# Kernel tuning notes

Measured on AMD Instinct MI355X. Metric: run time of the kernel, lower is better.

## Reference

```python
import jax, jax.numpy as jnp
import numpy as np

B, S, D = 2, 2048, 4096
H, KVH, HD = 32, 8, 128
ATTN_MULT = 0.08838834764831845
MAX_ATTN = 30.0
ROPE_THETA = 10000.0
MIN_MASKED = -65504.0  # large negative for masked logits


def setup_inputs() -> dict:
    key = jax.random.key(0)
    ks = jax.random.split(key, 5)
    hidden_states = jax.random.normal(ks[0], (B, S, D), dtype=jnp.float32)
    # boolean mask, True = masked (strictly upper triangular -> causal)
    attention_mask = jnp.triu(jnp.ones((S, S), dtype=bool), k=1)[None, None]
    position_ids = jnp.broadcast_to(jnp.arange(S, dtype=jnp.int64)[None], (B, S))
    sc = 0.02
    Wq = jax.random.normal(ks[1], (D, H * HD), dtype=jnp.float32) * sc
    Wk = jax.random.normal(ks[2], (D, KVH * HD), dtype=jnp.float32) * sc
    Wv = jax.random.normal(ks[3], (D, KVH * HD), dtype=jnp.float32) * sc
    Wo = jax.random.normal(ks[4], (H * HD, D), dtype=jnp.float32) * sc
    return {"hidden_states": hidden_states, "attention_mask": attention_mask,
            "position_ids": position_ids, "Wq": Wq, "Wk": Wk, "Wv": Wv, "Wo": Wo}


def _rotate_half(x):
    x1, x2 = jnp.split(x, 2, axis=-1)
    return jnp.concatenate([-x2, x1], axis=-1)


def _rope_cos_sin(position_ids):
    inv_freq = 1.0 / (ROPE_THETA ** (jnp.arange(0, HD, 2, dtype=jnp.float32) / HD))
    freqs = position_ids.astype(jnp.float32)[..., None] * inv_freq  # [B,S,HD/2]
    emb = jnp.concatenate([freqs, freqs], axis=-1)                  # [B,S,HD]
    return jnp.cos(emb)[:, None], jnp.sin(emb)[:, None]             # [B,1,S,HD]


def reference(hidden_states, attention_mask, position_ids, Wq, Wk, Wv, Wo):
    bsz, q_len, _ = hidden_states.shape
    q = (hidden_states @ Wq).reshape(bsz, q_len, H, HD).transpose(0, 2, 1, 3)
    k = (hidden_states @ Wk).reshape(bsz, q_len, KVH, HD).transpose(0, 2, 1, 3)
    v = (hidden_states @ Wv).reshape(bsz, q_len, KVH, HD).transpose(0, 2, 1, 3)

    cos, sin = _rope_cos_sin(position_ids)
    q = q * cos + _rotate_half(q) * sin
    k = k * cos + _rotate_half(k) * sin

    groups = H // KVH  # repeat_kv (GQA)
    k = jnp.repeat(k, groups, axis=1)
    v = jnp.repeat(v, groups, axis=1)

    w = jnp.einsum('bhqd,bhkd->bhqk', q, k).astype(jnp.float32)
    w = w * ATTN_MULT
    w = MAX_ATTN * jnp.tanh(w / MAX_ATTN)  # Grok-1 tanh soft-cap
    w = jnp.where(attention_mask, jnp.float32(MIN_MASKED), w)
    w = jax.nn.softmax(w, axis=-1).astype(q.dtype)

    out = jnp.einsum('bhqk,bhkd->bhqd', w, v)
    out = out.transpose(0, 2, 1, 3).reshape(bsz, q_len, H * HD)
    return out @ Wo
```

## Files before the change

### kernel.cpp

```cpp
#include <hip/hip_runtime.h>
#include <stdint.h>

#define B_ 2
#define S_ 2048
#define D_ 4096
#define H_ 32
#define KVH_ 8
#define HD_ 128
#define QKVN 6144
#define OHD 4096
#define ATTN_MULT 0.08838834764831845f
#define MAX_ATTN 30.0f

typedef __attribute__((ext_vector_type(8))) short short8;
typedef __attribute__((ext_vector_type(4))) float f32x4;

__device__ __forceinline__ unsigned short f2bf(float x) {
  union { float f; uint32_t u; } v; v.f = x;
  uint32_t r = v.u + 0x7FFFu + ((v.u >> 16) & 1u);
  return (unsigned short)(r >> 16);
}
__device__ __forceinline__ float bf2f(unsigned short h) {
  union { uint32_t u; float f; } v; v.u = ((uint32_t)h) << 16;
  return v.f;
}
__device__ __forceinline__ uint32_t packbf(float lo, float hi) {
  return (uint32_t)f2bf(lo) | ((uint32_t)f2bf(hi) << 16);
}

__global__ void k_cstab(float2* cs) {
  int idx = blockIdx.x * 256 + threadIdx.x;
  int d = idx & 63, s = idx >> 6;
  const float L2_10000 = 13.287712379549449f;
  float inv = exp2f(-(float)d * (L2_10000 / 64.0f));
  float f = (float)s * inv;
  cs[idx] = make_float2(cosf(f), sinf(f));
}

__global__ void k_cvt(const float* __restrict__ x, unsigned short* __restrict__ y, int n4) {
  int i = blockIdx.x * blockDim.x + threadIdx.x;
  int stride = gridDim.x * blockDim.x;
  for (; i < n4; i += stride) {
    float4 v = ((const float4*)x)[i];
    ushort4 o;
    o.x = f2bf(v.x); o.y = f2bf(v.y); o.z = f2bf(v.z); o.w = f2bf(v.w);
    ((ushort4*)y)[i] = o;
  }
}

__global__ void k_transpose(const float* __restrict__ W, unsigned short* __restrict__ WT,
                            int K, int N) {
  __shared__ float tile[32][33];
  int n0 = blockIdx.x * 32, k0 = blockIdx.y * 32;
  int tx = threadIdx.x, ty = threadIdx.y;
#pragma unroll
  for (int j = 0; j < 4; j++)
    tile[ty + j * 8][tx] = W[(size_t)(k0 + ty + j * 8) * N + n0 + tx];
  __syncthreads();
#pragma unroll
  for (int j = 0; j < 4; j++)
    WT[(size_t)(n0 + ty + j * 8) * K + k0 + tx] = f2bf(tile[tx][ty + j * 8]);
}

__global__ void k_rope(unsigned short* __restrict__ qkv, const float2* __restrict__ cs) {
  int row = blockIdx.x;
  int t = blockIdx.y * 256 + threadIdx.x;
  int head = t >> 6, d = t & 63;
  int col = head < H_ ? head * HD_ + d : D_ + (head - H_) * HD_ + d;
  unsigned short* p = qkv + (size_t)row * QKVN + col;
  int s = row & (S_ - 1);
  float2 c = cs[s * 64 + d];
  float x1 = bf2f(p[0]), x2 = bf2f(p[64]);
  p[0]  = f2bf(x1 * c.x - x2 * c.y);
  p[64] = f2bf(x2 * c.x + x1 * c.y);
}

template <bool OUT_BF16>
__global__ __launch_bounds__(256) void k_gemm(const unsigned short* __restrict__ A,
                                              const unsigned short* __restrict__ Bt,
                                              void* __restrict__ Cout,
                                              int M, int N, int K) {
  __shared__ unsigned short As[128 * 32];
  __shared__ unsigned short Bs[128 * 32];
  const int tid = threadIdx.x;
  const int wv = tid >> 6, lane = tid & 63;
  const int lg = lane >> 4, lq = lane & 15;
  const int bm = blockIdx.y * 128, bn = blockIdx.x * 128;
  const int wm = (wv >> 1) * 64, wn = (wv & 1) * 64;
  const int r0 = wv * 16 + (lane >> 2);
  const int kk = (lane & 3) * 8;

  f32x4 acc[4][4] = {};

  for (int k0 = 0; k0 < K; k0 += 32) {
#pragma unroll
    for (int p = 0; p < 2; p++) {
      int r = p * 64 + r0;
      __builtin_amdgcn_global_load_lds(
          (const __attribute__((address_space(1))) void*)(A + (size_t)(bm + r) * K + k0 + kk),
          (__attribute__((address_space(3))) void*)((char*)As + p * 4096 + wv * 1024),
          16, 0, 0);
      __builtin_amdgcn_global_load_lds(
          (const __attribute__((address_space(1))) void*)(Bt + (size_t)(bn + r) * K + k0 + kk),
          (__attribute__((address_space(3))) void*)((char*)Bs + p * 4096 + wv * 1024),
          16, 0, 0);
    }
    __syncthreads();
    short8 a[4], b[4];
#pragma unroll
    for (int f = 0; f < 4; f++) {
      a[f] = *(const short8*)&As[(wm + f * 16 + lq) * 32 + lg * 8];
      b[f] = *(const short8*)&Bs[(wn + f * 16 + lq) * 32 + lg * 8];
    }
#pragma unroll
    for (int i = 0; i < 4; i++)
#pragma unroll
      for (int j = 0; j < 4; j++)
        acc[i][j] = __builtin_amdgcn_mfma_f32_16x16x32_bf16(a[i], b[j], acc[i][j], 0, 0, 0);
    __syncthreads();
  }

#pragma unroll
  for (int i = 0; i < 4; i++)
#pragma unroll
    for (int j = 0; j < 4; j++) {
      int row = bm + wm + i * 16 + lg * 4;
      int col = bn + wn + j * 16 + lq;
#pragma unroll
      for (int t = 0; t < 4; t++) {
        float v = acc[i][j][t];
        if (OUT_BF16)
          ((unsigned short*)Cout)[(size_t)(row + t) * N + col] = f2bf(v);
        else
          ((float*)Cout)[(size_t)(row + t) * N + col] = v;
      }
    }
}

__device__ __forceinline__ float softcap(float s) {
  float x = s * (ATTN_MULT / MAX_ATTN);
  x = fminf(fmaxf(x, -15.f), 15.f);
  float e = __expf(2.0f * x);
  return MAX_ATTN * ((e - 1.0f) / (e + 1.0f));
}

__global__ __launch_bounds__(64) void k_attn(const unsigned short* __restrict__ qkv,
                                             unsigned short* __restrict__ out) {
  const int lane = threadIdx.x;
  const int lg = lane >> 4, lq = lane & 15;
  const int q0 = blockIdx.x * 32;
  const int h = blockIdx.y;
  const int b = blockIdx.z;
  const int kh = h >> 2;

  const unsigned short* Qb = qkv + (size_t)(b * S_) * QKVN + h * HD_;
  const unsigned short* Kb = qkv + (size_t)(b * S_) * QKVN + D_ + kh * HD_;
  const unsigned short* Vb = qkv + (size_t)(b * S_) * QKVN + D_ + KVH_ * HD_ + kh * HD_;

  short8 qf[2][4];
#pragma unroll
  for (int u = 0; u < 2; u++)
#pragma unroll
    for (int c = 0; c < 4; c++)
      qf[u][c] = *(const short8*)(Qb + (size_t)(q0 + u * 16 + lq) * QKVN + c * 32 + lg * 8);

  float m[2] = {-1e30f, -1e30f}, l[2] = {0.f, 0.f};
  f32x4 o[2][8] = {};

  const int kv_end = q0 + 32;
  for (int kv0 = 0; kv0 < kv_end; kv0 += 32) {
    short8 ka[2][4];
#pragma unroll
    for (int sI = 0; sI < 2; sI++)
#pragma unroll
      for (int c = 0; c < 4; c++)
        ka[sI][c] = *(const short8*)(Kb + (size_t)(kv0 + sI * 16 + lq) * QKVN + c * 32 + lg * 8);

    short8 vf[8];
#pragma unroll
    for (int fd = 0; fd < 8; fd++)
#pragma unroll
      for (int j = 0; j < 8; j++)
        vf[fd][j] = (short)Vb[(size_t)(kv0 + lg * 8 + j) * QKVN + fd * 16 + lq];

#pragma unroll
    for (int u = 0; u < 2; u++) {
      f32x4 stA = {}, stB = {};
#pragma unroll
      for (int c = 0; c < 4; c++) {
        stA = __builtin_amdgcn_mfma_f32_16x16x32_bf16(ka[0][c], qf[u][c], stA, 0, 0, 0);
        stB = __builtin_amdgcn_mfma_f32_16x16x32_bf16(ka[1][c], qf[u][c], stB, 0, 0, 0);
      }
      const int gq = q0 + u * 16 + lq;
      float w[8];
#pragma unroll
      for (int i = 0; i < 4; i++) {
        w[i]     = (kv0 + lg * 4 + i > gq)      ? -1e30f : softcap(stA[i]);
        w[4 + i] = (kv0 + 16 + lg * 4 + i > gq) ? -1e30f : softcap(stB[i]);
      }
      float mt = w[0];
#pragma unroll
      for (int i = 1; i < 8; i++) mt = fmaxf(mt, w[i]);
      mt = fmaxf(mt, __shfl_xor(mt, 16));
      mt = fmaxf(mt, __shfl_xor(mt, 32));
      float mnew = fmaxf(m[u], mt);
      float scale = __expf(m[u] - mnew);
      float p[8], ps = 0.f;
#pragma unroll
      for (int i = 0; i < 8; i++) { p[i] = __expf(w[i] - mnew); ps += p[i]; }
      ps += __shfl_xor(ps, 16);
      ps += __shfl_xor(ps, 32);
      l[u] = l[u] * scale + ps;
      m[u] = mnew;

      float sc[4];
#pragma unroll
      for (int t = 0; t < 4; t++)
        sc[t] = __shfl(scale, (lane & 48) + lg * 4 + t, 64);
#pragma unroll
      for (int fd = 0; fd < 8; fd++)
#pragma unroll
        for (int t = 0; t < 4; t++) o[u][fd][t] *= sc[t];

      uint32_t a01 = packbf(p[0], p[1]), a23 = packbf(p[2], p[3]);
      uint32_t b01 = packbf(p[4], p[5]), b23 = packbf(p[6], p[7]);
      int g0 = (lg & 1) << 1;
      int src0 = (g0 << 4) | lq;
      int src1 = ((g0 + 1) << 4) | lq;
      uint32_t wA0 = __shfl(a01, src0, 64), wB0 = __shfl(b01, src0, 64);
      uint32_t wA1 = __shfl(a23, src0, 64), wB1 = __shfl(b23, src0, 64);
      uint32_t wA2 = __shfl(a01, src1, 64), wB2 = __shfl(b01, src1, 64);
      uint32_t wA3 = __shfl(a23, src1, 64), wB3 = __shfl(b23, src1, 64);
      bool useB = lg >= 2;
      union { short8 v; uint32_t w4[4]; } pa;
      pa.w4[0] = useB ? wB0 : wA0;
      pa.w4[1] = useB ? wB1 : wA1;
      pa.w4[2] = useB ? wB2 : wA2;
      pa.w4[3] = useB ? wB3 : wA3;
#pragma unroll
      for (int fd = 0; fd < 8; fd++)
        o[u][fd] = __builtin_amdgcn_mfma_f32_16x16x32_bf16(pa.v, vf[fd], o[u][fd], 0, 0, 0);
    }
  }

#pragma unroll
  for (int u = 0; u < 2; u++) {
    float li[4];
#pragma unroll
    for (int t = 0; t < 4; t++)
      li[t] = __shfl(l[u], (lane & 48) + lg * 4 + t, 64);
#pragma unroll
    for (int fd = 0; fd < 8; fd++)
#pragma unroll
      for (int t = 0; t < 4; t++) {
        int row = q0 + u * 16 + lg * 4 + t;
        int col = h * HD_ + fd * 16 + lq;
        out[(size_t)(b * S_ + row) * OHD + col] = f2bf(o[u][fd][t] / li[t]);
      }
  }
}

extern "C" void kernel_launch(void* const* d_in, const int* in_sizes, int n_in,
                              void* d_out, int out_size, void* d_ws, size_t ws_size,
                              hipStream_t stream) {
  const float* hs = (const float*)d_in[0];
  const float* Wq = (const float*)d_in[3];
  const float* Wk = (const float*)d_in[4];
  const float* Wv = (const float*)d_in[5];
  const float* Wo = (const float*)d_in[6];

  char* ws = (char*)d_ws;
  unsigned short* WqkvT = (unsigned short*)ws;
  unsigned short* hsb   = (unsigned short*)(ws + 50331648);
  float2* cs            = (float2*)(ws + 50331648 + 33554432);
  unsigned short* qkv   = (unsigned short*)d_out;
  unsigned short* WoT   = WqkvT;
  unsigned short* attn  = hsb;

  k_cstab<<<dim3((S_ * 64) / 256), 256, 0, stream>>>(cs);
  k_transpose<<<dim3(4096 / 32, 4096 / 32), dim3(32, 8), 0, stream>>>(Wq, WqkvT, 4096, 4096);
  k_transpose<<<dim3(1024 / 32, 4096 / 32), dim3(32, 8), 0, stream>>>(Wk, WqkvT + (size_t)4096 * 4096, 4096, 1024);
  k_transpose<<<dim3(1024 / 32, 4096 / 32), dim3(32, 8), 0, stream>>>(Wv, WqkvT + (size_t)5120 * 4096, 4096, 1024);
  k_cvt<<<2048, 256, 0, stream>>>(hs, hsb, (B_ * S_ * D_) / 4);
  k_gemm<true><<<dim3(QKVN / 128, (B_ * S_) / 128), 256, 0, stream>>>(hsb, WqkvT, qkv, B_ * S_, QKVN, D_);
  k_rope<<<dim3(B_ * S_, 10), 256, 0, stream>>>(qkv, cs);
  k_transpose<<<dim3(4096 / 32, 4096 / 32), dim3(32, 8), 0, stream>>>(Wo, WoT, 4096, 4096);
  k_attn<<<dim3(S_ / 32, H_, B_), 64, 0, stream>>>(qkv, attn);
  k_gemm<false><<<dim3(D_ / 128, (B_ * S_) / 128), 256, 0, stream>>>(attn, WoT, d_out, B_ * S_, D_, D_);
}
```

Measured before the change: 1.287 ms.

## Transpose V for vector loads, use fixed softcap max, reverse causal block order

```diff
diff --git a/kernel.cpp b/kernel.cpp
--- a/kernel.cpp
+++ b/kernel.cpp
@@ -60,6 +60,22 @@
 #pragma unroll
   for (int j = 0; j < 4; j++)
     WT[(size_t)(n0 + ty + j * 8) * K + k0 + tx] = f2bf(tile[tx][ty + j * 8]);
+}
+
+__global__ void k_vt(const unsigned short* __restrict__ qkv, unsigned short* __restrict__ vT) {
+  __shared__ unsigned short tile[32][34];
+  int c0 = blockIdx.x * 32;
+  int s0 = blockIdx.y * 32;
+  int b  = blockIdx.z;
+  int tx = threadIdx.x, ty = threadIdx.y;
+#pragma unroll
+  for (int j = 0; j < 4; j++)
+    tile[ty + j * 8][tx] =
+        qkv[(size_t)(b * S_ + s0 + ty + j * 8) * QKVN + D_ + KVH_ * HD_ + c0 + tx];
+  __syncthreads();
+#pragma unroll
+  for (int j = 0; j < 4; j++)
+    vT[(size_t)(b * KVH_ * HD_ + c0 + ty + j * 8) * S_ + s0 + tx] = tile[tx][ty + j * 8];
 }
 
 __global__ void k_rope(unsigned short* __restrict__ qkv, const float2* __restrict__ cs) {
@@ -145,17 +161,18 @@
 }
 
 __global__ __launch_bounds__(64) void k_attn(const unsigned short* __restrict__ qkv,
+                                             const unsigned short* __restrict__ vT,
                                              unsigned short* __restrict__ out) {
   const int lane = threadIdx.x;
   const int lg = lane >> 4, lq = lane & 15;
-  const int q0 = blockIdx.x * 32;
+  const int q0 = (S_ / 32 - 1 - (int)blockIdx.x) * 32;
   const int h = blockIdx.y;
   const int b = blockIdx.z;
   const int kh = h >> 2;
 
   const unsigned short* Qb = qkv + (size_t)(b * S_) * QKVN + h * HD_;
   const unsigned short* Kb = qkv + (size_t)(b * S_) * QKVN + D_ + kh * HD_;
-  const unsigned short* Vb = qkv + (size_t)(b * S_) * QKVN + D_ + KVH_ * HD_ + kh * HD_;
+  const unsigned short* Vt = vT + (size_t)(b * KVH_ + kh) * HD_ * S_;
 
   short8 qf[2][4];
 #pragma unroll
@@ -164,7 +181,7 @@
     for (int c = 0; c < 4; c++)
       qf[u][c] = *(const short8*)(Qb + (size_t)(q0 + u * 16 + lq) * QKVN + c * 32 + lg * 8);
 
-  float m[2] = {-1e30f, -1e30f}, l[2] = {0.f, 0.f};
+  float l[2] = {0.f, 0.f};
   f32x4 o[2][8] = {};
 
   const int kv_end = q0 + 32;
@@ -179,9 +196,7 @@
     short8 vf[8];
 #pragma unroll
     for (int fd = 0; fd < 8; fd++)
-#pragma unroll
-      for (int j = 0; j < 8; j++)
-        vf[fd][j] = (short)Vb[(size_t)(kv0 + lg * 8 + j) * QKVN + fd * 16 + lq];
+      vf[fd] = *(const short8*)(Vt + (size_t)(fd * 16 + lq) * S_ + kv0 + lg * 8);
 
 #pragma unroll
     for (int u = 0; u < 2; u++) {
@@ -192,35 +207,19 @@
         stB = __builtin_amdgcn_mfma_f32_16x16x32_bf16(ka[1][c], qf[u][c], stB, 0, 0, 0);
       }
       const int gq = q0 + u * 16 + lq;
-      float w[8];
+      float p[8], ps = 0.f;
 #pragma unroll
       for (int i = 0; i < 4; i++) {
-        w[i]     = (kv0 + lg * 4 + i > gq)      ? -1e30f : softcap(stA[i]);
-        w[4 + i] = (kv0 + 16 + lg * 4 + i > gq) ? -1e30f : softcap(stB[i]);
-      }
-      float mt = w[0];
-#pragma unroll
-      for (int i = 1; i < 8; i++) mt = fmaxf(mt, w[i]);
-      mt = fmaxf(mt, __shfl_xor(mt, 16));
-      mt = fmaxf(mt, __shfl_xor(mt, 32));
-      float mnew = fmaxf(m[u], mt);
-      float scale = __expf(m[u] - mnew);
-      float p[8], ps = 0.f;
-#pragma unroll
-      for (int i = 0; i < 8; i++) { p[i] = __expf(w[i] - mnew); ps += p[i]; }
+        float wa = (kv0 + lg * 4 + i > gq)      ? -1e30f : softcap(stA[i]);
+        float wb = (kv0 + 16 + lg * 4 + i > gq) ? -1e30f : softcap(stB[i]);
+        p[i]     = __expf(wa - MAX_ATTN);
+        p[4 + i] = __expf(wb - MAX_ATTN);
+      }
+#pragma unroll
+      for (int i = 0; i < 8; i++) ps += p[i];
       ps += __shfl_xor(ps, 16);
       ps += __shfl_xor(ps, 32);
-      l[u] = l[u] * scale + ps;
-      m[u] = mnew;
-
-      float sc[4];
-#pragma unroll
-      for (int t = 0; t < 4; t++)
-        sc[t] = __shfl(scale, (lane & 48) + lg * 4 + t, 64);
-#pragma unroll
-      for (int fd = 0; fd < 8; fd++)
-#pragma unroll
-        for (int t = 0; t < 4; t++) o[u][fd][t] *= sc[t];
+      l[u] += ps;
 
       uint32_t a01 = packbf(p[0], p[1]), a23 = packbf(p[2], p[3]);
       uint32_t b01 = packbf(p[4], p[5]), b23 = packbf(p[6], p[7]);
@@ -274,6 +273,7 @@
   unsigned short* hsb   = (unsigned short*)(ws + 50331648);
   float2* cs            = (float2*)(ws + 50331648 + 33554432);
   unsigned short* qkv   = (unsigned short*)d_out;
+  unsigned short* vT    = (unsigned short*)((char*)d_out + 50331648);
   unsigned short* WoT   = WqkvT;
   unsigned short* attn  = hsb;
 
@@ -284,7 +284,8 @@
   k_cvt<<<2048, 256, 0, stream>>>(hs, hsb, (B_ * S_ * D_) / 4);
   k_gemm<true><<<dim3(QKVN / 128, (B_ * S_) / 128), 256, 0, stream>>>(hsb, WqkvT, qkv, B_ * S_, QKVN, D_);
   k_rope<<<dim3(B_ * S_, 10), 256, 0, stream>>>(qkv, cs);
+  k_vt<<<dim3(1024 / 32, S_ / 32, B_), dim3(32, 8), 0, stream>>>(qkv, vT);
   k_transpose<<<dim3(4096 / 32, 4096 / 32), dim3(32, 8), 0, stream>>>(Wo, WoT, 4096, 4096);
-  k_attn<<<dim3(S_ / 32, H_, B_), 64, 0, stream>>>(qkv, attn);
+  k_attn<<<dim3(S_ / 32, H_, B_), 64, 0, stream>>>(qkv, vT, attn);
   k_gemm<false><<<dim3(D_ / 128, (B_ * S_) / 128), 256, 0, stream>>>(attn, WoT, d_out, B_ * S_, D_, D_);
 }
```

Measured after the change: 1.161 ms. 1.11x faster.
